# Optimization experiments

Measured on AMD Instinct MI355X. Metric: run time of the kernel, lower is better.

## Reference

```python
import jax, jax.numpy as jnp
import numpy as np

B, N, F, D, H, S_OBJ, S_REG, ITERS = 32, 1024, 1152, 512, 8, 8, 4, 3
S = S_OBJ + S_REG
HD = D // H
SCALE = HD ** -0.5


def ln(x, g, b, eps=1e-5):
    m = x.mean(-1, keepdims=True)
    v = ((x - m) ** 2).mean(-1, keepdims=True)
    return (x - m) / jnp.sqrt(v + eps) * g + b


def setup_inputs() -> dict:
    key = jax.random.key(0)
    ks = jax.random.split(key, 16)
    s = 0.02
    d = {
        'features': jax.random.normal(ks[0], (B, N, F), jnp.float32),
        'noise': jax.random.normal(ks[1], (B, S, D), jnp.float32),
        'w_in': jax.random.normal(ks[2], (F, D), jnp.float32) * s,
        'b_in': jnp.zeros((D,), jnp.float32),
        'ln1_g': jnp.ones((D,), jnp.float32), 'ln1_b': jnp.zeros((D,), jnp.float32),
        'slot_mu': jax.random.normal(ks[3], (1, S, D), jnp.float32) * D ** -0.5,
        'slot_log_sigma': jnp.zeros((1, S, D), jnp.float32),
        'wq': jax.random.normal(ks[4], (D, D), jnp.float32) * s,
        'wk': jax.random.normal(ks[5], (D, D), jnp.float32) * s,
        'wv': jax.random.normal(ks[6], (D, D), jnp.float32) * s,
        'gru_wih': jax.random.normal(ks[7], (D, 3 * D), jnp.float32) * s,
        'gru_whh': jax.random.normal(ks[8], (D, 3 * D), jnp.float32) * s,
        'gru_bih': jnp.zeros((3 * D,), jnp.float32),
        'gru_bhh': jnp.zeros((3 * D,), jnp.float32),
        'nslots_g': jnp.ones((D,), jnp.float32), 'nslots_b': jnp.zeros((D,), jnp.float32),
        'ninput_g': jnp.ones((D,), jnp.float32), 'ninput_b': jnp.zeros((D,), jnp.float32),
        'ffn_ln_g': jnp.ones((D,), jnp.float32), 'ffn_ln_b': jnp.zeros((D,), jnp.float32),
        'ffn_w1': jax.random.normal(ks[9], (D, 4 * D), jnp.float32) * s,
        'ffn_b1': jnp.zeros((4 * D,), jnp.float32),
        'ffn_w2': jax.random.normal(ks[10], (4 * D, D), jnp.float32) * s,
        'ffn_b2': jnp.zeros((D,), jnp.float32),
        'sel_w1': jax.random.normal(ks[11], (D, D // 2), jnp.float32) * s,
        'sel_b1': jnp.zeros((D // 2,), jnp.float32),
        'sel_w2': jax.random.normal(ks[12], (D // 2, 2), jnp.float32) * s,
        'sel_b2': jnp.zeros((2,), jnp.float32),
    }
    return d


def reference(features, noise, w_in, b_in, ln1_g, ln1_b, slot_mu, slot_log_sigma,
              wq, wk, wv, gru_wih, gru_whh, gru_bih, gru_bhh,
              nslots_g, nslots_b, ninput_g, ninput_b,
              ffn_ln_g, ffn_ln_b, ffn_w1, ffn_b1, ffn_w2, ffn_b2,
              sel_w1, sel_b1, sel_w2, sel_b2):
    b = features.shape[0]
    # input_proj: Linear + LayerNorm, then norm_input LayerNorm
    x = ln(features @ w_in + b_in, ln1_g, ln1_b)
    inp = ln(x, ninput_g, ninput_b)
    slots = slot_mu + jnp.exp(slot_log_sigma) * noise  # [B,S,D]
    k = (inp @ wk).reshape(b, N, H, HD)
    v = (inp @ wv).reshape(b, N, H, HD)
    attn_out = None
    for _ in range(ITERS):
        sn = ln(slots, nslots_g, nslots_b)
        q = (sn @ wq).reshape(b, S, H, HD)
        dots = jnp.einsum('bihd,bjhd->bihj', q, k) * SCALE  # [B,S,H,N]
        # softmax over flattened (slot, head) axis per key j
        attn = jax.nn.softmax(dots.reshape(b, S * H, N), axis=1).reshape(b, S, H, N)
        attn_out = attn.mean(axis=2)  # [B,S,N]
        attn_n = (attn + 1e-8) / (attn.sum(axis=-1, keepdims=True) + 1e-8)
        upd = jnp.einsum('bjhd,bihj->bihd', v, attn_n).reshape(b * S, D)
        h = slots.reshape(b * S, D)
        gx = upd @ gru_wih + gru_bih
        gh = h @ gru_whh + gru_bhh
        xr, xz, xn = jnp.split(gx, 3, axis=-1)
        hr, hz, hn = jnp.split(gh, 3, axis=-1)
        r = jax.nn.sigmoid(xr + hr)
        z = jax.nn.sigmoid(xz + hz)
        n = jnp.tanh(xn + r * hn)
        slots = ((1.0 - z) * n + z * h).reshape(b, S, D)
        f = ln(slots, ffn_ln_g, ffn_ln_b)
        f = jax.nn.gelu(f @ ffn_w1 + ffn_b1, approximate=False) @ ffn_w2 + ffn_b2
        slots = slots + f
    obj = slots[:, :S_OBJ]  # [B,num_slots,D]
    logits = jax.nn.relu(obj @ sel_w1 + sel_b1) @ sel_w2 + sel_b2  # [B,num_slots,2]
    decision = (jnp.argmax(logits, axis=-1) == 1).astype(slots.dtype)
    # eval-mode repair: ensure >=2 active slots per row (deterministic: first inactive)
    needed = jnp.maximum(0.0, 2.0 - decision.sum(-1, keepdims=True))
    inactive_rank = jnp.cumsum(1.0 - decision, axis=-1)
    add = ((decision == 0) & (inactive_rank <= needed)).astype(decision.dtype)
    decision = decision + add
    obj = obj * decision[..., None]
    return obj, decision, attn_out[:, :S_OBJ]
```

## Files before the change

### kernel.cpp

```cpp
#include <hip/hip_runtime.h>
#include <math.h>

typedef __attribute__((ext_vector_type(8))) short short8;
typedef __attribute__((ext_vector_type(4))) float f32x4;

typedef const __attribute__((address_space(1))) void gv_t;
typedef __attribute__((address_space(3))) void lv_t;

__device__ __forceinline__ float b2f(short u) {
  union { unsigned int i; float f; } c; c.i = ((unsigned int)(unsigned short)u) << 16; return c.f;
}
__device__ __forceinline__ short f2b(float f) {
  union { float f; unsigned int i; } c; c.f = f;
  unsigned int r = c.i + 0x7FFFu + ((c.i >> 16) & 1u);
  return (short)(r >> 16);
}
__device__ __forceinline__ void glds(const short* g, short* l) {
  __builtin_amdgcn_global_load_lds((gv_t*)g, (lv_t*)l, 16, 0, 0);
}


__global__ __launch_bounds__(256) void k_prep(
    const float* __restrict__ w_in, const float* __restrict__ wk, const float* __restrict__ wv,
    const float* __restrict__ wq, const float* __restrict__ wih, const float* __restrict__ whh,
    const float* __restrict__ bih, const float* __restrict__ bhh,
    const float* __restrict__ w1, const float* __restrict__ w2, const float* __restrict__ sl1,
    const float* __restrict__ mu, const float* __restrict__ lsig, const float* __restrict__ noise,
    const float* __restrict__ features,
    short* __restrict__ Bt1, short* __restrict__ Btkv, short* __restrict__ wq_t,
    short* __restrict__ wgru, float* __restrict__ gbias,
    short* __restrict__ w1_t, short* __restrict__ w2_t, short* __restrict__ sl1_t,
    float* __restrict__ slots, short* __restrict__ gruA, short* __restrict__ Abf)
{
  int blk = blockIdx.x, t = threadIdx.x;
  if (blk >= 2168) {
    int idx = (blk-2168)*256 + t;
    const float4* p = (const float4*)(features + (size_t)idx * 8);
    float4 a = p[0], b = p[1];
    short8 r;
    r[0]=f2b(a.x); r[1]=f2b(a.y); r[2]=f2b(a.z); r[3]=f2b(a.w);
    r[4]=f2b(b.x); r[5]=f2b(b.y); r[6]=f2b(b.z); r[7]=f2b(b.w);
    *(short8*)(Abf + (size_t)idx*8) = r;
  } else if (blk < 1392) {
    __shared__ float tile[64][68];
    int id = blk;
    const float* src = nullptr; short* dst; int Kd, n0, k0, sld = 0, sr0 = 0, sc0 = 0;
    if (id < 144) {
      dst = Bt1; Kd = 1152; n0 = (id/18)*64; k0 = (id%18)*64;
      src = w_in; sld = 512; sr0 = k0; sc0 = n0;
    } else if (id < 272) {
      id -= 144; dst = Btkv; Kd = 512; n0 = (id/8)*64; k0 = (id%8)*64;
      src = (n0 < 512) ? wk : wv; sld = 512; sr0 = k0; sc0 = n0 & 511;
    } else if (id < 336) {
      id -= 272; dst = wq_t; Kd = 512; n0 = (id/8)*64; k0 = (id%8)*64;
      src = wq; sld = 512; sr0 = k0; sc0 = n0;
    } else if (id < 848) {
      id -= 336; dst = wgru; Kd = 1024; n0 = (id/16)*64; k0 = (id%16)*64;
      int g = n0 >> 9, c0 = n0 & 511; bool hi = (k0 >= 512);
      sld = 1536; sr0 = hi ? k0 - 512 : k0;
      if (g == 0)      { src = hi ? whh : wih; sc0 = c0; }
      else if (g == 1) { src = hi ? whh : wih; sc0 = 512 + c0; }
      else if (g == 2) { src = hi ? nullptr : wih; sc0 = 1024 + c0; }
      else             { src = hi ? whh : nullptr; sc0 = 1024 + c0; }
    } else if (id < 1104) {
      id -= 848; dst = w1_t; Kd = 512; n0 = (id/8)*64; k0 = (id%8)*64;
      src = w1; sld = 2048; sr0 = k0; sc0 = n0;
    } else if (id < 1360) {
      id -= 1104; dst = w2_t; Kd = 2048; n0 = (id/32)*64; k0 = (id%32)*64;
      src = w2; sld = 512; sr0 = k0; sc0 = n0;
    } else {
      id -= 1360; dst = sl1_t; Kd = 512; n0 = (id/8)*64; k0 = (id%8)*64;
      src = sl1; sld = 256; sr0 = k0; sc0 = n0;
    }
    if (src) {
      #pragma unroll
      for (int i = 0; i < 4; ++i) {
        int kk = (t >> 4) + i*16, nn = (t & 15) * 4;
        *(float4*)&tile[kk][nn] = *(const float4*)(src + (size_t)(sr0+kk)*sld + sc0 + nn);
      }
    } else {
      #pragma unroll
      for (int i = 0; i < 4; ++i) {
        int kk = (t >> 4) + i*16, nn = (t & 15) * 4;
        tile[kk][nn] = 0.f; tile[kk][nn+1] = 0.f; tile[kk][nn+2] = 0.f; tile[kk][nn+3] = 0.f;
      }
    }
    __syncthreads();
    #pragma unroll
    for (int i = 0; i < 2; ++i) {
      int c = i*256 + t;
      int row = c >> 3, off = (c & 7) * 8;
      short8 o;
      #pragma unroll
      for (int e = 0; e < 8; ++e) o[e] = f2b(tile[off+e][row]);
      *(short8*)(dst + (size_t)(n0+row)*Kd + k0 + off) = o;
    }
  } else if (blk < 1400) {
    int n = (blk-1392)*256 + t;
    int g = n >> 9;
    float v;
    if (g <= 1)      v = bih[n] + bhh[n];
    else if (g == 2) v = bih[n];
    else             v = bhh[1024 + (n - 1536)];
    gbias[n] = v;
  } else {
    int idx = (blk-1400)*256 + t;
    int sd = idx % 6144;
    float v = mu[sd] + __expf(lsig[sd]) * noise[idx];
    slots[idx] = v;
    int row = idx >> 9, c = idx & 511;
    gruA[(size_t)row*1024 + 512 + c] = f2b(v);
  }
}


__global__ __launch_bounds__(256) void gemm_p(
    const short* __restrict__ A, const short* __restrict__ Bt,
    const float* __restrict__ bias, short* __restrict__ Cb,
    int N, int K, int lda, int ldb)
{
  __shared__ short As[2][128*64];
  __shared__ short Bs[2][128*64];
  const int t = threadIdx.x;
  const int lane = t & 63, wave = t >> 6;

  const int nwg = gridDim.x, gridX = N >> 7, orig = blockIdx.x;
  const int q = nwg >> 3, r = nwg & 7, xcd = orig & 7, base = orig >> 3;
  const int wgid = (xcd < r ? xcd*(q+1) : r*(q+1) + (xcd - r)*q) + base;
  const int bx = wgid % gridX, by = wgid / gridX;

  const int rowBase = by * 128, colBase = bx * 128;
  const int wm = (wave >> 1) * 64, wn = (wave & 1) * 64;
  const int fr = lane & 15, kcf = lane >> 4;
  f32x4 acc[4][4] = {};

  int srow[4], scol[4];
  #pragma unroll
  for (int i = 0; i < 4; ++i) {
    int c = i*256 + t;
    srow[i] = c >> 3;
    scol[i] = ((c & 7) ^ (srow[i] & 7)) * 8;
  }

  const int nsteps = K >> 6;
  auto STAGE = [&](int step, int buf) {
    int kb = step * 64;
    #pragma unroll
    for (int i = 0; i < 4; ++i) {
      int c = i*256 + t;
      glds(A + (size_t)(rowBase + srow[i])*lda + kb + scol[i], As[buf] + c*8);
      glds(Bt + (size_t)(colBase + srow[i])*ldb + kb + scol[i], Bs[buf] + c*8);
    }
  };

  STAGE(0, 0);
  if (nsteps > 1) { STAGE(1, 1); asm volatile("s_waitcnt vmcnt(8)" ::: "memory"); }
  else            {              asm volatile("s_waitcnt vmcnt(0)" ::: "memory"); }
  __builtin_amdgcn_sched_barrier(0);
  __builtin_amdgcn_s_barrier();
  __builtin_amdgcn_sched_barrier(0);

  for (int tt = 0; tt < nsteps; ++tt) {
    const int cur = tt & 1;
    short8 af[2][4], bf[2][4];
    #pragma unroll
    for (int ks = 0; ks < 2; ++ks) {
      int kc = ks*4 + kcf;
      #pragma unroll
      for (int m = 0; m < 4; ++m) {
        int rowa = wm + m*16 + fr;
        af[ks][m] = *(const short8*)(As[cur] + rowa*64 + (kc ^ (rowa & 7))*8);
        int rowb = wn + m*16 + fr;
        bf[ks][m] = *(const short8*)(Bs[cur] + rowb*64 + (kc ^ (rowb & 7))*8);
      }
    }
    asm volatile("s_waitcnt lgkmcnt(0)" ::: "memory");
    __builtin_amdgcn_sched_barrier(0);
    __builtin_amdgcn_s_barrier();
    __builtin_amdgcn_sched_barrier(0);
    if (tt + 2 < nsteps) STAGE(tt + 2, cur);
    #pragma unroll
    for (int ks = 0; ks < 2; ++ks)
      #pragma unroll
      for (int m = 0; m < 4; ++m)
        #pragma unroll
        for (int n = 0; n < 4; ++n)
          acc[m][n] = __builtin_amdgcn_mfma_f32_16x16x32_bf16(af[ks][m], bf[ks][n], acc[m][n], 0, 0, 0);
    if (tt + 1 < nsteps) {
      if (tt + 2 < nsteps) asm volatile("s_waitcnt vmcnt(8)" ::: "memory");
      else                 asm volatile("s_waitcnt vmcnt(0)" ::: "memory");
      __builtin_amdgcn_sched_barrier(0);
      __builtin_amdgcn_s_barrier();
      __builtin_amdgcn_sched_barrier(0);
    }
  }

  const int cr = (lane >> 4) * 4, cc2 = lane & 15;
  #pragma unroll
  for (int m = 0; m < 4; ++m)
    #pragma unroll
    for (int n = 0; n < 4; ++n) {
      int col = colBase + wn + n*16 + cc2;
      float bv = bias ? bias[col] : 0.f;
      #pragma unroll
      for (int j = 0; j < 4; ++j) {
        int row = rowBase + wm + m*16 + cr + j;
        Cb[(size_t)row*N + col] = f2b(acc[m][n][j] + bv);
      }
    }
}


template<int ACT, bool OUTBF, bool SPLITK>
__global__ __launch_bounds__(256) void gemm_t(
    const short* __restrict__ A, const short* __restrict__ Bt,
    const float* __restrict__ bias,
    float* __restrict__ Cf, short* __restrict__ Cb,
    int N, int Kp, int lda, int ldb, int ldf, int ldcb, int cboff, int skstride)
{
  __shared__ short As[128*64];
  __shared__ short Bs[128*64];
  const int t = threadIdx.x;
  const int lane = t & 63, wave = t >> 6;

  const int nwg = gridDim.x, gridX = N >> 7, orig = blockIdx.x;
  const int q = nwg >> 3, r = nwg & 7, xcd = orig & 7, base = orig >> 3;
  const int wgid = (xcd < r ? xcd*(q+1) : r*(q+1) + (xcd - r)*q) + base;
  const int bx = wgid % gridX, by = wgid / gridX;

  const int rowBase = by * 128, colBase = bx * 128;
  const size_t koff = (size_t)blockIdx.y * Kp;
  const int wm = (wave >> 1) * 64, wn = (wave & 1) * 64;
  const int fr = lane & 15, kcf = lane >> 4;
  f32x4 acc[4][4] = {};

  int srow[4], scol[4];
  #pragma unroll
  for (int i = 0; i < 4; ++i) {
    int c = i*256 + t;
    srow[i] = c >> 3;
    scol[i] = ((c & 7) ^ (srow[i] & 7)) * 8;
  }

  for (int kb = 0; kb < Kp; kb += 64) {
    __syncthreads();
    #pragma unroll
    for (int i = 0; i < 4; ++i) {
      int c = i*256 + t;
      glds(A + (size_t)(rowBase + srow[i])*lda + koff + kb + scol[i], As + c*8);
      glds(Bt + (size_t)(colBase + srow[i])*ldb + koff + kb + scol[i], Bs + c*8);
    }
    __syncthreads();
    #pragma unroll
    for (int ks = 0; ks < 2; ++ks) {
      short8 af[4], bf[4];
      #pragma unroll
      for (int m = 0; m < 4; ++m) {
        int row = wm + m*16 + fr;
        int kc = ks*4 + kcf;
        af[m] = *(const short8*)(As + row*64 + (kc ^ (row & 7))*8);
      }
      #pragma unroll
      for (int n = 0; n < 4; ++n) {
        int row = wn + n*16 + fr;
        int kc = ks*4 + kcf;
        bf[n] = *(const short8*)(Bs + row*64 + (kc ^ (row & 7))*8);
      }
      #pragma unroll
      for (int m = 0; m < 4; ++m)
        #pragma unroll
        for (int n = 0; n < 4; ++n)
          acc[m][n] = __builtin_amdgcn_mfma_f32_16x16x32_bf16(af[m], bf[n], acc[m][n], 0, 0, 0);
    }
  }

  const int cr = (lane >> 4) * 4, cc2 = lane & 15;
  if (SPLITK) {
    float* dst = Cf + (size_t)blockIdx.y * skstride;
    #pragma unroll
    for (int m = 0; m < 4; ++m)
      #pragma unroll
      for (int n = 0; n < 4; ++n) {
        int col = colBase + wn + n*16 + cc2;
        #pragma unroll
        for (int j = 0; j < 4; ++j) {
          int row = rowBase + wm + m*16 + cr + j;
          dst[(size_t)row * ldf + col] = acc[m][n][j];
        }
      }
  } else {
    #pragma unroll
    for (int m = 0; m < 4; ++m)
      #pragma unroll
      for (int n = 0; n < 4; ++n) {
        int col = colBase + wn + n*16 + cc2;
        float bv = bias ? bias[col] : 0.f;
        #pragma unroll
        for (int j = 0; j < 4; ++j) {
          int row = rowBase + wm + m*16 + cr + j;
          float v = acc[m][n][j] + bv;
          if (ACT == 1) v = 0.5f*v*(1.f + erff(v*0.70710678118f));
          else if (ACT == 2) v = fmaxf(v, 0.f);
          if (OUTBF) Cb[(size_t)row*ldcb + cboff + col] = f2b(v);
          else Cf[(size_t)row*ldf + col] = v;
        }
      }
  }
}


__global__ __launch_bounds__(256) void k_gruln(const float* __restrict__ p, const float* __restrict__ gbias,
    float* __restrict__ slots, short* __restrict__ fln,
    const float* __restrict__ g, const float* __restrict__ bb)
{
  int t = threadIdx.x, lane = t & 63;
  int row = blockIdx.x*4 + (t >> 6);
  int c = lane * 8;
  float g0[8], g1[8], g2[8], g3[8];
  *(float4*)g0     = *(const float4*)(gbias + c);
  *(float4*)(g0+4) = *(const float4*)(gbias + c + 4);
  *(float4*)g1     = *(const float4*)(gbias + 512 + c);
  *(float4*)(g1+4) = *(const float4*)(gbias + 512 + c + 4);
  *(float4*)g2     = *(const float4*)(gbias + 1024 + c);
  *(float4*)(g2+4) = *(const float4*)(gbias + 1024 + c + 4);
  *(float4*)g3     = *(const float4*)(gbias + 1536 + c);
  *(float4*)(g3+4) = *(const float4*)(gbias + 1536 + c + 4);
  const float* base = p + (size_t)row*2048 + c;
  #pragma unroll
  for (int s = 0; s < 4; ++s) {
    const float* qq = base + (size_t)s*786432;
    #pragma unroll
    for (int gi = 0; gi < 4; ++gi) {
      float* dst = (gi == 0) ? g0 : (gi == 1) ? g1 : (gi == 2) ? g2 : g3;
      float4 a = *(const float4*)(qq + gi*512), b4 = *(const float4*)(qq + gi*512 + 4);
      dst[0]+=a.x; dst[1]+=a.y; dst[2]+=a.z; dst[3]+=a.w;
      dst[4]+=b4.x; dst[5]+=b4.y; dst[6]+=b4.z; dst[7]+=b4.w;
    }
  }
  float hold[8], v[8];
  *(float4*)hold     = *(const float4*)(slots + (size_t)row*512 + c);
  *(float4*)(hold+4) = *(const float4*)(slots + (size_t)row*512 + c + 4);
  #pragma unroll
  for (int e = 0; e < 8; ++e) {
    float r = 1.f/(1.f+__expf(-g0[e]));
    float z = 1.f/(1.f+__expf(-g1[e]));
    float n = tanhf(g2[e] + r*g3[e]);
    v[e] = (1.f-z)*n + z*hold[e];
  }
  *(float4*)(slots + (size_t)row*512 + c)     = *(float4*)v;
  *(float4*)(slots + (size_t)row*512 + c + 4) = *(float4*)(v+4);
  float s1 = 0.f, s2 = 0.f;
  #pragma unroll
  for (int e = 0; e < 8; ++e) { s1 += v[e]; s2 += v[e]*v[e]; }
  #pragma unroll
  for (int m = 1; m < 64; m <<= 1) { s1 += __shfl_xor(s1, m, 64); s2 += __shfl_xor(s2, m, 64); }
  float mean = s1 * (1.f/512.f);
  float rs = rsqrtf(s2*(1.f/512.f) - mean*mean + 1e-5f);
  short8 o;
  #pragma unroll
  for (int e = 0; e < 8; ++e) o[e] = f2b((v[e]-mean)*rs*g[c+e] + bb[c+e]);
  *(short8*)(fln + (size_t)row*512 + c) = o;
}


__global__ __launch_bounds__(256) void k_ffn2redln(const float* __restrict__ p, const float* __restrict__ b2,
    float* __restrict__ slots, short* __restrict__ gruA, short* __restrict__ sn,
    const float* __restrict__ g, const float* __restrict__ bb)
{
  int t = threadIdx.x, lane = t & 63;
  int row = blockIdx.x*4 + (t >> 6);
  int c = lane * 8;
  size_t base = (size_t)row*512 + c;
  float v[8];
  *(float4*)v     = *(const float4*)(slots + base);
  *(float4*)(v+4) = *(const float4*)(slots + base + 4);
  #pragma unroll
  for (int e = 0; e < 8; ++e) v[e] += b2[c+e];
  #pragma unroll
  for (int s = 0; s < 8; ++s) {
    const float* qq = p + (size_t)s*196608 + base;
    float4 a = *(const float4*)qq, b4 = *(const float4*)(qq+4);
    v[0]+=a.x; v[1]+=a.y; v[2]+=a.z; v[3]+=a.w;
    v[4]+=b4.x; v[5]+=b4.y; v[6]+=b4.z; v[7]+=b4.w;
  }
  *(float4*)(slots + base)     = *(float4*)v;
  *(float4*)(slots + base + 4) = *(float4*)(v+4);
  short8 o;
  #pragma unroll
  for (int e = 0; e < 8; ++e) o[e] = f2b(v[e]);
  *(short8*)(gruA + (size_t)row*1024 + 512 + c) = o;
  float s1 = 0.f, s2 = 0.f;
  #pragma unroll
  for (int e = 0; e < 8; ++e) { s1 += v[e]; s2 += v[e]*v[e]; }
  #pragma unroll
  for (int m = 1; m < 64; m <<= 1) { s1 += __shfl_xor(s1, m, 64); s2 += __shfl_xor(s2, m, 64); }
  float mean = s1 * (1.f/512.f);
  float rs = rsqrtf(s2*(1.f/512.f) - mean*mean + 1e-5f);
  short8 o2;
  #pragma unroll
  for (int e = 0; e < 8; ++e) o2[e] = f2b((v[e]-mean)*rs*g[c+e] + bb[c+e]);
  *(short8*)(sn + base) = o2;
}


__global__ __launch_bounds__(256) void k_ffn1red(const float* __restrict__ p, const float* __restrict__ b1,
                                                 short* __restrict__ f1) {
  int i = blockIdx.x*256 + threadIdx.x;
  int col = (i*8) & 2047;
  float v[8], w[8];
  *(float4*)v = *(const float4*)(p + (size_t)i*8);
  *(float4*)(v+4) = *(const float4*)(p + (size_t)i*8 + 4);
  const float* p2 = p + 786432;
  *(float4*)w = *(const float4*)(p2 + (size_t)i*8);
  *(float4*)(w+4) = *(const float4*)(p2 + (size_t)i*8 + 4);
  short8 o;
  #pragma unroll
  for (int e = 0; e < 8; ++e) {
    float x = v[e] + w[e] + b1[col + e];
    x = 0.5f*x*(1.f + erff(x*0.70710678118f));
    o[e] = f2b(x);
  }
  *(short8*)(f1 + (size_t)i*8) = o;
}


__global__ __launch_bounds__(256) void k_ln2(const short* __restrict__ y, short* __restrict__ inp,
    const float* __restrict__ g1, const float* __restrict__ b1,
    const float* __restrict__ g2, const float* __restrict__ b2)
{
  int t = threadIdx.x, lane = t & 63;
  int row = blockIdx.x * 4 + (t >> 6);
  const short8 raw = *(const short8*)(y + (size_t)row*512 + lane*8);
  float x[8];
  #pragma unroll
  for (int e = 0; e < 8; ++e) x[e] = b2f(raw[e]);
  float s = 0.f, ss = 0.f;
  #pragma unroll
  for (int e = 0; e < 8; ++e) { s += x[e]; ss += x[e]*x[e]; }
  #pragma unroll
  for (int m = 1; m < 64; m <<= 1) { s += __shfl_xor(s, m, 64); ss += __shfl_xor(ss, m, 64); }
  float mean = s * (1.f/512.f);
  float rs = rsqrtf(ss*(1.f/512.f) - mean*mean + 1e-5f);
  int c = lane * 8;
  #pragma unroll
  for (int e = 0; e < 8; ++e) x[e] = (x[e]-mean)*rs*g1[c+e] + b1[c+e];
  s = 0.f; ss = 0.f;
  #pragma unroll
  for (int e = 0; e < 8; ++e) { s += x[e]; ss += x[e]*x[e]; }
  #pragma unroll
  for (int m = 1; m < 64; m <<= 1) { s += __shfl_xor(s, m, 64); ss += __shfl_xor(ss, m, 64); }
  float mean2 = s * (1.f/512.f);
  float rs2 = rsqrtf(ss*(1.f/512.f) - mean2*mean2 + 1e-5f);
  short8 o;
  #pragma unroll
  for (int e = 0; e < 8; ++e) o[e] = f2b((x[e]-mean2)*rs2*g2[c+e] + b2[c+e]);
  *(short8*)(inp + (size_t)row*512 + lane*8) = o;
}


__global__ __launch_bounds__(256) void k_lnb(const float* __restrict__ x, short* __restrict__ out,
    const float* __restrict__ g, const float* __restrict__ b)
{
  int t = threadIdx.x, lane = t & 63;
  int row = blockIdx.x * 4 + (t >> 6);
  const float* src = x + (size_t)row*512 + lane*8;
  float v[8];
  *(float4*)v = *(const float4*)src;
  *(float4*)(v+4) = *(const float4*)(src+4);
  float s = 0.f, ss = 0.f;
  #pragma unroll
  for (int e = 0; e < 8; ++e) { s += v[e]; ss += v[e]*v[e]; }
  #pragma unroll
  for (int m = 1; m < 64; m <<= 1) { s += __shfl_xor(s, m, 64); ss += __shfl_xor(ss, m, 64); }
  float mean = s * (1.f/512.f);
  float rs = rsqrtf(ss*(1.f/512.f) - mean*mean + 1e-5f);
  int c = lane * 8;
  short8 o;
  #pragma unroll
  for (int e = 0; e < 8; ++e) o[e] = f2b((v[e]-mean)*rs*g[c+e] + b[c+e]);
  *(short8*)(out + (size_t)row*512 + c) = o;
}


__global__ __launch_bounds__(256) void k_attn(
    const float* __restrict__ qparts, const short* __restrict__ kv,
    float* __restrict__ pvp, float* __restrict__ denp, float* __restrict__ aout)
{
  __shared__ float qs[12][512];
  __shared__ float ksh[128][65];
  __shared__ float dots[96][132];
  const int t = threadIdx.x;
  const int jt = blockIdx.x, b = blockIdx.y;

  for (int i = t; i < 6144; i += 256) {
    int s = i >> 9, d = i & 511;
    size_t o = (size_t)(b*12+s)*512 + d;
    qs[s][d] = qparts[o] + qparts[196608 + o] + qparts[393216 + o] + qparts[589824 + o];
  }

  const int jj = t & 127, sg = t >> 7;
  for (int h = 0; h < 8; ++h) {
    __syncthreads();
    #pragma unroll
    for (int i = 0; i < 4; ++i) {
      int c = i*256 + t;
      int j2 = c >> 3, seg = (c & 7) * 8;
      short8 raw = *(const short8*)(kv + ((size_t)(b*1024 + jt*128 + j2))*1024 + h*64 + seg);
      #pragma unroll
      for (int e = 0; e < 8; ++e) ksh[j2][seg+e] = b2f(raw[e]);
    }
    __syncthreads();
    float d6[6] = {};
    for (int d = 0; d < 64; ++d) {
      float kvv = ksh[jj][d];
      #pragma unroll
      for (int i = 0; i < 6; ++i) d6[i] += qs[sg*6+i][h*64+d] * kvv;
    }
    #pragma unroll
    for (int i = 0; i < 6; ++i) dots[(sg*6+i)*8 + h][jj] = d6[i] * 0.125f;
  }
  __syncthreads();

  {
    int j = t >> 1, half = (t & 1) * 48;
    float mx = -1e30f;
    #pragma unroll
    for (int i = 0; i < 48; ++i) mx = fmaxf(mx, dots[half+i][j]);
    mx = fmaxf(mx, __shfl_xor(mx, 1, 64));
    float ex[48];
    float sum = 0.f;
    #pragma unroll
    for (int i = 0; i < 48; ++i) { ex[i] = __expf(dots[half+i][j] - mx); sum += ex[i]; }
    sum += __shfl_xor(sum, 1, 64);
    float inv = 1.f / sum;
    float as_[6] = {0,0,0,0,0,0};
    #pragma unroll
    for (int i = 0; i < 48; ++i) {
      float a = ex[i] * inv;
      dots[half+i][j] = a;
      as_[i >> 3] += a;
    }
    if (aout) {
      int sbase = (t & 1) * 6;
      #pragma unroll
      for (int q2 = 0; q2 < 6; ++q2) {
        int s = sbase + q2;
        if (s < 8) aout[((size_t)(b*8+s))*1024 + jt*128 + j] = as_[q2] * 0.125f;
      }
    }
  }

  const int d = t & 63, sq = t >> 6;
  for (int h = 0; h < 8; ++h) {
    __syncthreads();
    #pragma unroll
    for (int i = 0; i < 4; ++i) {
      int c = i*256 + t;
      int j2 = c >> 3, seg = (c & 7) * 8;
      short8 raw = *(const short8*)(kv + ((size_t)(b*1024 + jt*128 + j2))*1024 + 512 + h*64 + seg);
      #pragma unroll
      for (int e = 0; e < 8; ++e) ksh[j2][seg+e] = b2f(raw[e]);
    }
    __syncthreads();
    float a3[3] = {0.f, 0.f, 0.f};
    for (int j2 = 0; j2 < 128; ++j2) {
      float vv = ksh[j2][d];
      #pragma unroll
      for (int i = 0; i < 3; ++i) a3[i] += dots[(sq + 4*i)*8 + h][j2] * vv;
    }
    #pragma unroll
    for (int i = 0; i < 3; ++i)
      pvp[((size_t)(jt*32+b))*6144 + (sq + 4*i)*512 + h*64 + d] = a3[i];
    if (t < 12) {
      float ls = 0.f;
      for (int j2 = 0; j2 < 128; ++j2) ls += dots[t*8 + h][j2];
      denp[((size_t)(jt*32+b))*96 + t*8 + h] = ls;
    }
  }
}


__global__ __launch_bounds__(256) void k_pvred(const float* __restrict__ pvp, const float* __restrict__ denp,
                                               short* __restrict__ gruA)
{
  __shared__ float den[96];
  int t = threadIdx.x, b = blockIdx.x;
  if (t < 96) {
    float s = 0.f;
    #pragma unroll
    for (int jt2 = 0; jt2 < 8; ++jt2) s += denp[((size_t)(jt2*32+b))*96 + t];
    den[t] = s + 1e-8f;
  }
  __syncthreads();
  for (int i = t; i < 6144; i += 256) {
    int s = i >> 9, rem = i & 511, h = rem >> 6;
    float acc = 0.f;
    #pragma unroll
    for (int jt2 = 0; jt2 < 8; ++jt2) acc += pvp[((size_t)(jt2*32+b))*6144 + i];
    gruA[((size_t)(b*12+s))*1024 + rem] = f2b(acc / den[s*8 + h]);
  }
}


__global__ __launch_bounds__(64) void k_decide(const float* __restrict__ hid, const float* __restrict__ w2,
    const float* __restrict__ b2, const float* __restrict__ slots, float* __restrict__ out)
{
  __shared__ float lg[16];
  __shared__ float dec[8];
  int b = blockIdx.x, t = threadIdx.x;
  if (t < 16) {
    int s = t >> 1, cl = t & 1;
    const float* hr = hid + (size_t)(b*12+s)*256;
    float a = b2[cl];
    for (int k = 0; k < 256; ++k) a += hr[k] * w2[k*2+cl];
    lg[t] = a;
  }
  __syncthreads();
  if (t == 0) {
    float d0[8]; float tot = 0.f;
    #pragma unroll
    for (int s = 0; s < 8; ++s) { d0[s] = (lg[2*s+1] > lg[2*s]) ? 1.f : 0.f; tot += d0[s]; }
    float needed = fmaxf(0.f, 2.f - tot);
    float cum = 0.f;
    #pragma unroll
    for (int s = 0; s < 8; ++s) {
      cum += 1.f - d0[s];
      float add = (d0[s] == 0.f && cum <= needed) ? 1.f : 0.f;
      float dd = d0[s] + add;
      dec[s] = dd;
      out[131072 + b*8 + s] = dd;
    }
  }
  __syncthreads();
  for (int i = 0; i < 64; ++i) {
    int idx = i*64 + t;
    int s = idx >> 9, c = idx & 511;
    out[(size_t)(b*8+s)*512 + c] = slots[(size_t)(b*12+s)*512 + c] * dec[s];
  }
}


extern "C" void kernel_launch(void* const* d_in, const int* in_sizes, int n_in,
                              void* d_out, int out_size, void* d_ws, size_t ws_size,
                              hipStream_t stream) {
  const float* features = (const float*)d_in[0];
  const float* noise    = (const float*)d_in[1];
  const float* w_in     = (const float*)d_in[2];
  const float* b_in     = (const float*)d_in[3];
  const float* ln1_g    = (const float*)d_in[4];
  const float* ln1_b    = (const float*)d_in[5];
  const float* slot_mu  = (const float*)d_in[6];
  const float* slot_ls  = (const float*)d_in[7];
  const float* wq       = (const float*)d_in[8];
  const float* wk       = (const float*)d_in[9];
  const float* wv       = (const float*)d_in[10];
  const float* gru_wih  = (const float*)d_in[11];
  const float* gru_whh  = (const float*)d_in[12];
  const float* gru_bih  = (const float*)d_in[13];
  const float* gru_bhh  = (const float*)d_in[14];
  const float* nslots_g = (const float*)d_in[15];
  const float* nslots_b = (const float*)d_in[16];
  const float* ninput_g = (const float*)d_in[17];
  const float* ninput_b = (const float*)d_in[18];
  const float* ffnln_g  = (const float*)d_in[19];
  const float* ffnln_b  = (const float*)d_in[20];
  const float* ffn_w1   = (const float*)d_in[21];
  const float* ffn_b1   = (const float*)d_in[22];
  const float* ffn_w2   = (const float*)d_in[23];
  const float* ffn_b2   = (const float*)d_in[24];
  const float* sel_w1   = (const float*)d_in[25];
  const float* sel_b1   = (const float*)d_in[26];
  const float* sel_w2   = (const float*)d_in[27];
  const float* sel_b2   = (const float*)d_in[28];
  float* out = (float*)d_out;
  float* fnull = (float*)nullptr;
  short* snull = (short*)nullptr;

  char* w = (char*)d_ws;
  size_t off = 0;
  auto alloc = [&](size_t n) { char* p = w + off; off = (off + n + 255) & ~255ULL; return p; };
  short* Abf   = (short*)alloc(75497472);
  short* kv    = Abf;
  short* ybf   = (short*)alloc(33554432);
  short* inp   = (short*)alloc(33554432);
  short* Bt1   = (short*)alloc(1179648);
  short* Btkv  = (short*)alloc(1048576);
  short* wq_t  = (short*)alloc(524288);
  short* wgru  = (short*)alloc(4194304);
  float* gbias = (float*)alloc(8192);
  short* w1_t  = (short*)alloc(2097152);
  short* w2_t  = (short*)alloc(2097152);
  short* sl1_t = (short*)alloc(262144);
  float* slots = (float*)alloc(786432);
  short* gruA  = (short*)alloc(786432);
  short* sn    = (short*)alloc(393216);
  float* parts = (float*)alloc(12582912);
  float* pvp   = (float*)alloc(6291456);
  float* denp  = (float*)alloc(98304);
  short* fln   = (short*)alloc(393216);
  short* f1    = (short*)alloc(1572864);
  float* hid   = (float*)alloc(393216);
  (void)ws_size; (void)in_sizes; (void)n_in; (void)out_size;

  k_prep<<<dim3(20600), dim3(256), 0, stream>>>(
      w_in, wk, wv, wq, gru_wih, gru_whh, gru_bih, gru_bhh,
      ffn_w1, ffn_w2, sel_w1, slot_mu, slot_ls, noise, features,
      Bt1, Btkv, wq_t, wgru, gbias, w1_t, w2_t, sl1_t, slots, gruA, Abf);

  gemm_p<<<dim3(1024), dim3(256), 0, stream>>>(Abf, Bt1, b_in, ybf, 512, 1152, 1152, 1152);
  k_ln2<<<dim3(8192), dim3(256), 0, stream>>>(ybf, inp, ln1_g, ln1_b, ninput_g, ninput_b);
  gemm_p<<<dim3(2048), dim3(256), 0, stream>>>(inp, Btkv, fnull, kv, 1024, 512, 512, 512);

  k_lnb<<<dim3(96), dim3(256), 0, stream>>>(slots, sn, nslots_g, nslots_b);

  for (int it = 0; it < 3; ++it) {
    gemm_t<0,false,true><<<dim3(12, 4), dim3(256), 0, stream>>>(
        sn, wq_t, fnull, parts, snull, 512, 128, 512, 512, 512, 0, 0, 196608);
    k_attn<<<dim3(8, 32), dim3(256), 0, stream>>>(parts, kv, pvp, denp,
        it == 2 ? out + 131328 : fnull);
    k_pvred<<<dim3(32), dim3(256), 0, stream>>>(pvp, denp, gruA);
    gemm_t<0,false,true><<<dim3(48, 4), dim3(256), 0, stream>>>(
        gruA, wgru, fnull, parts, snull, 2048, 256, 1024, 1024, 2048, 0, 0, 786432);
    k_gruln<<<dim3(96), dim3(256), 0, stream>>>(parts, gbias, slots, fln, ffnln_g, ffnln_b);
    gemm_t<0,false,true><<<dim3(48, 2), dim3(256), 0, stream>>>(
        fln, w1_t, fnull, parts, snull, 2048, 256, 512, 512, 2048, 0, 0, 786432);
    k_ffn1red<<<dim3(384), dim3(256), 0, stream>>>(parts, ffn_b1, f1);
    gemm_t<0,false,true><<<dim3(12, 8), dim3(256), 0, stream>>>(
        f1, w2_t, fnull, parts, snull, 512, 256, 2048, 2048, 512, 0, 0, 196608);
    k_ffn2redln<<<dim3(96), dim3(256), 0, stream>>>(parts, ffn_b2, slots, gruA, sn,
        nslots_g, nslots_b);
  }

  gemm_t<2,false,false><<<dim3(6), dim3(256), 0, stream>>>(
      gruA + 512, sl1_t, sel_b1, hid, snull, 256, 512, 1024, 512, 256, 0, 0, 0);
  k_decide<<<dim3(32), dim3(64), 0, stream>>>(hid, sel_w2, sel_b2, slots, out);
}
```

Before: 520.3 us.

## Double-buffer K/V tiles in attention via async global-to-LDS loads with XOR swizzle

In the attention kernel, the K and V tiles for each head are now staged as bf16 directly into LDS using global_load_lds, with double buffering so the next head's tile is prefetched while the current head is computed. An XOR swizzle on the 16-byte segments is meant to avoid bank conflicts on reads, and conversion to float now happens at use time. The aim is to hide global memory latency and drop the register round trip and float conversion during staging. In exchange it relies on hand-written waitcnt and barrier sequencing, which is fragile, and LDS use rises for the two bf16 buffers of K and V.

```diff
diff --git a/kernel.cpp b/kernel.cpp
--- a/kernel.cpp
+++ b/kernel.cpp
@@ -487,10 +487,31 @@
     float* __restrict__ pvp, float* __restrict__ denp, float* __restrict__ aout)
 {
   __shared__ float qs[12][512];
-  __shared__ float ksh[128][65];
+  __shared__ short kbf[2][128*64];
+  __shared__ short vbf[2][128*64];
   __shared__ float dots[96][132];
   const int t = threadIdx.x;
   const int jt = blockIdx.x, b = blockIdx.y;
+  const short* kvb = kv + ((size_t)(b*1024 + jt*128))*1024;
+
+  auto stageK = [&](int h, int buf) {
+    #pragma unroll
+    for (int i = 0; i < 4; ++i) {
+      int c = i*256 + t;
+      int j2 = c >> 3, d0 = c & 7;
+      glds(kvb + (size_t)j2*1024 + h*64 + ((d0 ^ (j2 & 7))*8), kbf[buf] + c*8);
+    }
+  };
+  auto stageV = [&](int h, int buf) {
+    #pragma unroll
+    for (int i = 0; i < 4; ++i) {
+      int c = i*256 + t;
+      int j2 = c >> 3, d0 = c & 7;
+      glds(kvb + (size_t)j2*1024 + 512 + h*64 + ((d0 ^ (j2 & 7))*8), vbf[buf] + c*8);
+    }
+  };
+
+  stageK(0, 0);
 
   for (int i = t; i < 6144; i += 256) {
     int s = i >> 9, d = i & 511;
@@ -500,26 +521,31 @@
 
   const int jj = t & 127, sg = t >> 7;
   for (int h = 0; h < 8; ++h) {
-    __syncthreads();
-    #pragma unroll
-    for (int i = 0; i < 4; ++i) {
-      int c = i*256 + t;
-      int j2 = c >> 3, seg = (c & 7) * 8;
-      short8 raw = *(const short8*)(kv + ((size_t)(b*1024 + jt*128 + j2))*1024 + h*64 + seg);
-      #pragma unroll
-      for (int e = 0; e < 8; ++e) ksh[j2][seg+e] = b2f(raw[e]);
-    }
-    __syncthreads();
+    if (h < 7) stageK(h+1, (h+1)&1);
+    else       stageV(0, 0);
+    asm volatile("s_waitcnt vmcnt(4) lgkmcnt(0)" ::: "memory");
+    __builtin_amdgcn_sched_barrier(0);
+    __builtin_amdgcn_s_barrier();
+    __builtin_amdgcn_sched_barrier(0);
+    const short* kb = kbf[h & 1];
     float d6[6] = {};
-    for (int d = 0; d < 64; ++d) {
-      float kvv = ksh[jj][d];
-      #pragma unroll
-      for (int i = 0; i < 6; ++i) d6[i] += qs[sg*6+i][h*64+d] * kvv;
+    #pragma unroll
+    for (int g = 0; g < 8; ++g) {
+      short8 kk = *(const short8*)(kb + jj*64 + ((g ^ (jj & 7))*8));
+      #pragma unroll
+      for (int e = 0; e < 8; ++e) {
+        float kd = b2f(kk[e]);
+        #pragma unroll
+        for (int i = 0; i < 6; ++i) d6[i] += qs[sg*6+i][h*64 + g*8 + e] * kd;
+      }
     }
     #pragma unroll
     for (int i = 0; i < 6; ++i) dots[(sg*6+i)*8 + h][jj] = d6[i] * 0.125f;
-  }
-  __syncthreads();
+    asm volatile("s_waitcnt lgkmcnt(0)" ::: "memory");
+    __builtin_amdgcn_sched_barrier(0);
+    __builtin_amdgcn_s_barrier();
+    __builtin_amdgcn_sched_barrier(0);
+  }
 
   {
     int j = t >> 1, half = (t & 1) * 48;
@@ -549,22 +575,23 @@
       }
     }
   }
+  asm volatile("s_waitcnt lgkmcnt(0)" ::: "memory");
+  __builtin_amdgcn_sched_barrier(0);
+  __builtin_amdgcn_s_barrier();
+  __builtin_amdgcn_sched_barrier(0);
 
   const int d = t & 63, sq = t >> 6;
+  const int gch = d >> 3, ech = d & 7;
   for (int h = 0; h < 8; ++h) {
-    __syncthreads();
-    #pragma unroll
-    for (int i = 0; i < 4; ++i) {
-      int c = i*256 + t;
-      int j2 = c >> 3, seg = (c & 7) * 8;
-      short8 raw = *(const short8*)(kv + ((size_t)(b*1024 + jt*128 + j2))*1024 + 512 + h*64 + seg);
-      #pragma unroll
-      for (int e = 0; e < 8; ++e) ksh[j2][seg+e] = b2f(raw[e]);
-    }
-    __syncthreads();
+    if (h < 7) { stageV(h+1, (h+1)&1); asm volatile("s_waitcnt vmcnt(4)" ::: "memory"); }
+    else       {                        asm volatile("s_waitcnt vmcnt(0)" ::: "memory"); }
+    __builtin_amdgcn_sched_barrier(0);
+    __builtin_amdgcn_s_barrier();
+    __builtin_amdgcn_sched_barrier(0);
+    const short* vb = vbf[h & 1];
     float a3[3] = {0.f, 0.f, 0.f};
     for (int j2 = 0; j2 < 128; ++j2) {
-      float vv = ksh[j2][d];
+      float vv = b2f(vb[j2*64 + ((gch ^ (j2 & 7))*8) + ech]);
       #pragma unroll
       for (int i = 0; i < 3; ++i) a3[i] += dots[(sq + 4*i)*8 + h][j2] * vv;
     }
@@ -576,6 +603,9 @@
       for (int j2 = 0; j2 < 128; ++j2) ls += dots[t*8 + h][j2];
       denp[((size_t)(jt*32+b))*96 + t*8 + h] = ls;
     }
+    __builtin_amdgcn_sched_barrier(0);
+    __builtin_amdgcn_s_barrier();
+    __builtin_amdgcn_sched_barrier(0);
   }
 }
 
```

Result: slower. 536.7 us (+3.2%).
